# Kernel tuning notes

Measured on AMD Instinct MI355X. Metric: run time of the kernel, lower is better.

## Reference

```python
import jax, jax.numpy as jnp
import numpy as np

N = 50000          # nodes
E = 640000         # edges (before self-loops)
DIM_FEATS = 128
DIM_H = 32
HEADS1 = 8
NUM_CLASS = 16
NEG_SLOPE_ATT = 0.2   # PyG GATv2Conv default negative_slope
NEG_SLOPE_OUT = 0.01  # F.leaky_relu default


def setup_inputs() -> dict:
    key = jax.random.key(0)
    ks = jax.random.split(key, 12)
    s = 0.1
    x = jax.random.normal(ks[0], (N, DIM_FEATS), dtype=jnp.float32)
    edge_index = jax.random.randint(ks[1], (2, E), 0, N, dtype=jnp.int32)
    # GATv2Conv layer 1: dim_feats -> dim_h per head, 8 heads, concat
    W1l = jax.random.normal(ks[2], (DIM_FEATS, HEADS1 * DIM_H), dtype=jnp.float32) * s
    W1r = jax.random.normal(ks[3], (DIM_FEATS, HEADS1 * DIM_H), dtype=jnp.float32) * s
    att1 = jax.random.normal(ks[4], (HEADS1, DIM_H), dtype=jnp.float32) * s
    b1 = jnp.zeros((HEADS1 * DIM_H,), dtype=jnp.float32)
    # GATv2Conv layer 2: 256 -> num_class, 1 head, concat=False
    W2l = jax.random.normal(ks[5], (HEADS1 * DIM_H, NUM_CLASS), dtype=jnp.float32) * s
    W2r = jax.random.normal(ks[6], (HEADS1 * DIM_H, NUM_CLASS), dtype=jnp.float32) * s
    att2 = jax.random.normal(ks[7], (1, NUM_CLASS), dtype=jnp.float32) * s
    b2 = jnp.zeros((NUM_CLASS,), dtype=jnp.float32)
    return {"x": x, "edge_index": edge_index, "W1l": W1l, "W1r": W1r,
            "att1": att1, "b1": b1, "W2l": W2l, "W2r": W2r,
            "att2": att2, "b2": b2}


def _segment_softmax(scores, seg, num_segments):
    # scores: [E, H], seg: [E] destination node ids
    m = jax.ops.segment_max(scores, seg, num_segments=num_segments)  # [N, H]
    e = jnp.exp(scores - m[seg])
    denom = jax.ops.segment_sum(e, seg, num_segments=num_segments)   # [N, H]
    return e / (denom[seg] + 1e-16)


def _gatv2_layer(x, src, dst, Wl, Wr, att, bias, heads, out_ch, concat):
    n = x.shape[0]
    xl = (x @ Wl).reshape(n, heads, out_ch)  # source transform
    xr = (x @ Wr).reshape(n, heads, out_ch)  # target transform
    # per-edge GATv2 score: a^T LeakyReLU(xl[j] + xr[i])
    e = jax.nn.leaky_relu(xl[src] + xr[dst], negative_slope=NEG_SLOPE_ATT)  # [E,H,F]
    alpha = jnp.einsum('ehf,hf->eh', e, att)                                # [E,H]
    alpha = _segment_softmax(alpha, dst, n)
    msg = xl[src] * alpha[:, :, None]                                       # [E,H,F]
    out = jax.ops.segment_sum(msg, dst, num_segments=n)                     # [N,H,F]
    out = out.reshape(n, heads * out_ch) if concat else out.mean(axis=1)
    return out + bias


def reference(x, edge_index, W1l, W1r, att1, b1, W2l, W2r, att2, b2):
    # add_self_loops=True (PyG GATv2Conv default)
    loop = jnp.arange(N, dtype=edge_index.dtype)
    src = jnp.concatenate([edge_index[0], loop])
    dst = jnp.concatenate([edge_index[1], loop])
    # eval mode: all dropouts are identity
    h = _gatv2_layer(x, src, dst, W1l, W1r, att1, b1, HEADS1, DIM_H, concat=True)
    h = jax.nn.elu(h)
    h = _gatv2_layer(h, src, dst, W2l, W2r, att2, b2, 1, NUM_CLASS, concat=False)
    return jax.nn.leaky_relu(h, negative_slope=NEG_SLOPE_OUT)
```

## Files before the change

kernel.cpp:

```cpp
#include <hip/hip_runtime.h>
#include <math.h>

#define NN 50000
#define E0 640000
#define ET 690000
#define F1 128
#define D1 256
#define C2 16
#define NB 196
#define MPAD 50048
#define PADK 136
#define LOG2E 1.4426950408889634f
#define NBK1 782

typedef _Float16 f16x8 __attribute__((ext_vector_type(8)));
typedef _Float16 h2 __attribute__((ext_vector_type(2)));
typedef __attribute__((ext_vector_type(4))) float f32x4;

__device__ __forceinline__ unsigned short f2h(float f) {
  union { _Float16 h; unsigned short u; } c;
  c.h = (_Float16)f;
  return c.u;
}
__device__ __forceinline__ float h2f(unsigned short u) {
  union { unsigned short u; _Float16 h; } c; c.u = u; return (float)c.h;
}
__device__ __forceinline__ h2 u2h2(unsigned u) {
  union { unsigned u; h2 h; } c; c.u = u; return c.h;
}
__device__ __forceinline__ unsigned h22u(h2 h) {
  union { h2 h; unsigned u; } c; c.h = h; return c.u;
}

__global__ __launch_bounds__(256) void k_prep(
    const float* __restrict__ Wl, const float* __restrict__ Wr,
    const float* __restrict__ W2l, const float* __restrict__ W2r,
    const int* __restrict__ ei,
    unsigned short* __restrict__ wt, unsigned short* __restrict__ wt2,
    int* __restrict__ deg) {
  const int b = blockIdx.x;
  if (b < 256) {
    int tid = b * 256 + threadIdx.x;
    int n = tid >> 7, k = tid & 127;
    float v = (n < 256) ? Wl[k * 256 + n] : Wr[k * 256 + (n - 256)];
    wt[tid] = f2h(v);
  } else if (b < 288) {
    int tid = (b - 256) * 256 + threadIdx.x;
    int n = tid >> 8, k = tid & 255;
    float v = (n < 16) ? W2l[k * 16 + n] : W2r[k * 16 + (n - 16)];
    wt2[tid] = f2h(v);
  } else {
    int e = (b - 288) * 256 + threadIdx.x;
    if (e >= ET) return;
    int d = (e < E0) ? ei[E0 + e] : (e - E0);
    atomicAdd(&deg[d], 1);
  }
}

__global__ __launch_bounds__(256) void k_gemm1m(
    const float* __restrict__ x, const unsigned short* __restrict__ wt,
    unsigned short* __restrict__ xlh, unsigned short* __restrict__ xrh) {
  __shared__ unsigned short Al[128 * PADK];
  __shared__ unsigned short Bl[128 * PADK];
  const int t = threadIdx.x;
  const int m0 = blockIdx.x * 128;
  const int n0 = blockIdx.y * 128;
  {
    const int r = t >> 4;
    const int c = (t & 15) * 8;
#pragma unroll
    for (int p = 0; p < 8; ++p) {
      const int row = r + p * 16;
      const int rg = m0 + row;
      const float* xp = &x[(size_t)(rg < NN ? rg : NN - 1) * F1 + c];
      float4 lo = *(const float4*)xp;
      float4 hi = *(const float4*)(xp + 4);
      h2 q0 = h2{(_Float16)lo.x, (_Float16)lo.y};
      h2 q1 = h2{(_Float16)lo.z, (_Float16)lo.w};
      h2 q2 = h2{(_Float16)hi.x, (_Float16)hi.y};
      h2 q3 = h2{(_Float16)hi.z, (_Float16)hi.w};
      uint4 st; st.x = h22u(q0); st.y = h22u(q1); st.z = h22u(q2); st.w = h22u(q3);
      *(uint4*)&Al[row * PADK + c] = st;
      *(float4*)&Bl[row * PADK + c] = *(const float4*)&wt[(size_t)(n0 + row) * F1 + c];
    }
  }
  __syncthreads();
  const int wave = t >> 6, lane = t & 63;
  const int mw = (wave >> 1) * 64, nw = (wave & 1) * 64;
  const int fr = lane & 15, fq = lane >> 4;
  f32x4 acc[4][4] = {};
#pragma unroll
  for (int ks = 0; ks < 4; ++ks) {
    const int ko = ks * 32 + fq * 8;
    f16x8 a[4], b[4];
#pragma unroll
    for (int i = 0; i < 4; ++i)
      a[i] = *(const f16x8*)&Al[(mw + i * 16 + fr) * PADK + ko];
#pragma unroll
    for (int j = 0; j < 4; ++j)
      b[j] = *(const f16x8*)&Bl[(nw + j * 16 + fr) * PADK + ko];
#pragma unroll
    for (int i = 0; i < 4; ++i)
#pragma unroll
      for (int j = 0; j < 4; ++j)
        acc[i][j] = __builtin_amdgcn_mfma_f32_16x16x32_f16(a[i], b[j], acc[i][j], 0, 0, 0);
  }
  unsigned short* outp = (n0 < 256) ? xlh : xrh;
  const int cb = (n0 & 255) + nw + fr;
#pragma unroll
  for (int j = 0; j < 4; ++j) {
    const int col = cb + j * 16;
    const int head = col >> 5, f = col & 31;
    unsigned short* hp = outp + (size_t)head * NN * 32 + f;
#pragma unroll
    for (int i = 0; i < 4; ++i) {
      const int gm0 = m0 + mw + i * 16 + fq * 4;
#pragma unroll
      for (int r = 0; r < 4; ++r) {
        const int gm = gm0 + r;
        if (gm < NN) hp[(size_t)gm * 32] = f2h(acc[i][j][r]);
      }
    }
  }
}

__global__ __launch_bounds__(256) void k_scan_part(const int* __restrict__ deg,
                                                   int* __restrict__ part) {
  int i = blockIdx.x * 256 + threadIdx.x;
  int v = (i < NN) ? deg[i] : 0;
  v += __shfl_xor(v, 1);  v += __shfl_xor(v, 2);  v += __shfl_xor(v, 4);
  v += __shfl_xor(v, 8);  v += __shfl_xor(v, 16); v += __shfl_xor(v, 32);
  __shared__ int w[4];
  if ((threadIdx.x & 63) == 0) w[threadIdx.x >> 6] = v;
  __syncthreads();
  if (threadIdx.x == 0) part[blockIdx.x] = w[0] + w[1] + w[2] + w[3];
}

__global__ __launch_bounds__(256) void k_scan_apply(int* __restrict__ deg,
                                                    const int* __restrict__ part,
                                                    int* __restrict__ offs) {
  __shared__ int lds[256];
  __shared__ int red[4];
  const int b = blockIdx.x, t = threadIdx.x;
  const int i = b * 256 + t;
  int v = (i < NN) ? deg[i] : 0;
  lds[t] = v;
  int pp = 0;
  for (int j = t; j < b; j += 256) pp += part[j];
  pp += __shfl_xor(pp, 1);  pp += __shfl_xor(pp, 2);  pp += __shfl_xor(pp, 4);
  pp += __shfl_xor(pp, 8);  pp += __shfl_xor(pp, 16); pp += __shfl_xor(pp, 32);
  if ((t & 63) == 0) red[t >> 6] = pp;
  __syncthreads();
  const int prefix = red[0] + red[1] + red[2] + red[3];
  for (int off = 1; off < 256; off <<= 1) {
    int u = (t >= off) ? lds[t - off] : 0;
    __syncthreads();
    lds[t] += u;
    __syncthreads();
  }
  int excl = prefix + lds[t] - v;
  if (i < NN) { offs[i] = excl; deg[i] = excl; }
  if (b == NB - 1 && t == 255) offs[NN] = prefix + lds[255];
}

__global__ void k_scatter(const int* __restrict__ ei, int* __restrict__ cur,
                          unsigned short* __restrict__ csr) {
  int e = blockIdx.x * 256 + threadIdx.x;
  if (e >= ET) return;
  int s, d;
  if (e < E0) { s = ei[e]; d = ei[E0 + e]; } else { s = d = e - E0; }
  int pos = atomicAdd(&cur[d], 1);
  csr[pos] = (unsigned short)s;
}

__global__ __launch_bounds__(256) void k_agg1(
    const unsigned short* __restrict__ xlh, const unsigned short* __restrict__ xrh,
    unsigned short* __restrict__ hb,
    const int* __restrict__ offs, const unsigned short* __restrict__ csr,
    const float* __restrict__ att, const float* __restrict__ b1) {
  const int b = blockIdx.x;
  const int head = b & 7;
  const int wave = threadIdx.x >> 6;
  const int lane = threadIdx.x & 63;
  const int g = lane >> 2;
  const int j4 = lane & 3;
  const int n = (b >> 3) * 64 + wave * 16 + g;
  const bool valid = n < NN;
  const int colh = j4 * 8;
  const int col = head * 32 + colh;
  const unsigned short* xlhead = xlh + (size_t)head * NN * 32;

  const int nc = valid ? n : 0;
  const uint4 xru = *(const uint4*)&xrh[((size_t)head * NN + nc) * 32 + colh];
  h2 xr2[4];
  xr2[0] = u2h2(xru.x); xr2[1] = u2h2(xru.y);
  xr2[2] = u2h2(xru.z); xr2[3] = u2h2(xru.w);
  float at8[8];
  *(float4*)&at8[0] = *(const float4*)&att[col];
  *(float4*)&at8[4] = *(const float4*)&att[col + 4];
  h2 ath6[4], ath4[4];
#pragma unroll
  for (int j = 0; j < 4; ++j) {
    ath6[j] = h2{(_Float16)(at8[2 * j] * (0.6f * LOG2E)),
                 (_Float16)(at8[2 * j + 1] * (0.6f * LOG2E))};
    ath4[j] = h2{(_Float16)(at8[2 * j] * (0.4f * LOG2E)),
                 (_Float16)(at8[2 * j + 1] * (0.4f * LOG2E))};
  }
  float l = 0.f;
  h2 acc2[4] = {h2{0, 0}, h2{0, 0}, h2{0, 0}, h2{0, 0}};
  const int beg = valid ? offs[n] : 0;
  const int fin = valid ? offs[n + 1] : 0;

  auto score = [&](const h2* xh) -> float {
    float cv = 0.f, ca = 0.f;
#pragma unroll
    for (int j = 0; j < 4; ++j) {
      h2 v = xh[j] + xr2[j];
      h2 a = u2h2(h22u(v) & 0x7FFF7FFFu);
      cv = __builtin_amdgcn_fdot2(v, ath6[j], cv, false);
      ca = __builtin_amdgcn_fdot2(a, ath4[j], ca, false);
    }
    float c = cv + ca;
    c += __shfl_xor(c, 1);
    c += __shfl_xor(c, 2);
    return c;
  };

  int idx = beg;
  for (; idx + 1 < fin; idx += 2) {
    const int s0 = csr[idx], s1 = csr[idx + 1];
    const uint4 w0 = *(const uint4*)&xlhead[(size_t)s0 * 32 + colh];
    const uint4 w1 = *(const uint4*)&xlhead[(size_t)s1 * 32 + colh];
    h2 xh0[4], xh1[4];
    xh0[0] = u2h2(w0.x); xh0[1] = u2h2(w0.y); xh0[2] = u2h2(w0.z); xh0[3] = u2h2(w0.w);
    xh1[0] = u2h2(w1.x); xh1[1] = u2h2(w1.y); xh1[2] = u2h2(w1.z); xh1[3] = u2h2(w1.w);
    const float c0 = score(xh0);
    const float c1 = score(xh1);
    const float p0 = exp2f(c0), p1 = exp2f(c1);
    l += p0 + p1;
    const _Float16 p0h = (_Float16)p0, p1h = (_Float16)p1;
    const h2 p02 = h2{p0h, p0h}, p12 = h2{p1h, p1h};
#pragma unroll
    for (int j = 0; j < 4; ++j) acc2[j] += p02 * xh0[j] + p12 * xh1[j];
  }
  if (idx < fin) {
    const int s0 = csr[idx];
    const uint4 w0 = *(const uint4*)&xlhead[(size_t)s0 * 32 + colh];
    h2 xh0[4];
    xh0[0] = u2h2(w0.x); xh0[1] = u2h2(w0.y); xh0[2] = u2h2(w0.z); xh0[3] = u2h2(w0.w);
    const float c0 = score(xh0);
    const float p0 = exp2f(c0);
    l += p0;
    const _Float16 p0h = (_Float16)p0;
    const h2 p02 = h2{p0h, p0h};
#pragma unroll
    for (int j = 0; j < 4; ++j) acc2[j] += p02 * xh0[j];
  }
  if (valid) {
    const float rl = 1.f / (l + 1e-16f);
    float b8[8], o[8];
    *(float4*)&b8[0] = *(const float4*)&b1[col];
    *(float4*)&b8[4] = *(const float4*)&b1[col + 4];
#pragma unroll
    for (int j = 0; j < 4; ++j) {
      o[2 * j]     = (float)acc2[j][0] * rl + b8[2 * j];
      o[2 * j + 1] = (float)acc2[j][1] * rl + b8[2 * j + 1];
    }
#pragma unroll
    for (int k = 0; k < 8; ++k) o[k] = o[k] > 0.f ? o[k] : expm1f(o[k]);
    ushort4 p;
    p.x = f2h(o[0]); p.y = f2h(o[1]); p.z = f2h(o[2]); p.w = f2h(o[3]);
    ushort4 q;
    q.x = f2h(o[4]); q.y = f2h(o[5]); q.z = f2h(o[6]); q.w = f2h(o[7]);
    uint4 packed;
    packed.x = *(unsigned*)&p.x; packed.y = *(unsigned*)&p.z;
    packed.z = *(unsigned*)&q.x; packed.w = *(unsigned*)&q.z;
    *(uint4*)&hb[(size_t)n * D1 + col] = packed;
  }
}

__global__ __launch_bounds__(256) void k_gemm2m(
    const unsigned short* __restrict__ hb, const unsigned short* __restrict__ wt2,
    unsigned short* __restrict__ h2lh, float* __restrict__ h2r) {
  const int t = threadIdx.x;
  const int wave = t >> 6, lane = t & 63;
  const int fr = lane & 15, fq = lane >> 4;
  const int m0 = blockIdx.x * 128 + wave * 32;
  f32x4 acc[2][2] = {};
#pragma unroll
  for (int ks = 0; ks < 8; ++ks) {
    const int ko = ks * 32 + fq * 8;
    f16x8 a[2], b[2];
#pragma unroll
    for (int i = 0; i < 2; ++i) {
      int row = m0 + i * 16 + fr; if (row >= NN) row = NN - 1;
      a[i] = *(const f16x8*)&hb[(size_t)row * D1 + ko];
    }
#pragma unroll
    for (int j = 0; j < 2; ++j)
      b[j] = *(const f16x8*)&wt2[(j * 16 + fr) * 256 + ko];
#pragma unroll
    for (int i = 0; i < 2; ++i)
#pragma unroll
      for (int j = 0; j < 2; ++j)
        acc[i][j] = __builtin_amdgcn_mfma_f32_16x16x32_f16(a[i], b[j], acc[i][j], 0, 0, 0);
  }
#pragma unroll
  for (int i = 0; i < 2; ++i) {
    const int gm0 = m0 + i * 16 + fq * 4;
#pragma unroll
    for (int r = 0; r < 4; ++r) {
      const int gm = gm0 + r;
      if (gm < NN) {
        h2lh[(size_t)gm * C2 + fr] = f2h(acc[i][0][r]);
        h2r[(size_t)gm * C2 + fr] = acc[i][1][r];
      }
    }
  }
}

__global__ __launch_bounds__(256) void k_agg2(
    const unsigned short* __restrict__ h2lh, const float* __restrict__ h2r,
    const int* __restrict__ offs, const unsigned short* __restrict__ csr,
    const float* __restrict__ att2, const float* __restrict__ b2,
    float* __restrict__ out) {
  const int wave = threadIdx.x >> 6;
  const int lane = threadIdx.x & 63;
  const int n = blockIdx.x * 4 + wave;
  if (n >= NN) return;
  const int c = lane & 15, g = lane >> 4;
  const float xr_v = h2r[(size_t)n * C2 + c];
  const float att_v = att2[c] * LOG2E;
  float l = 0.f, acc = 0.f;
  const int beg = offs[n], fin = offs[n + 1];
  for (int idx = beg + g; idx < fin; idx += 4) {
    int s = csr[idx];
    float xlv = h2f(h2lh[(size_t)s * C2 + c]);
    float v = xlv + xr_v;
    v = fmaxf(v, 0.2f * v);
    float sc0 = v * att_v;
    sc0 += __shfl_xor(sc0, 1);
    sc0 += __shfl_xor(sc0, 2);
    sc0 += __shfl_xor(sc0, 4);
    sc0 += __shfl_xor(sc0, 8);
    float p = exp2f(sc0);
    l += p;
    acc = fmaf(p, xlv, acc);
  }
  l += __shfl_xor(l, 16);   l += __shfl_xor(l, 32);
  acc += __shfl_xor(acc, 16); acc += __shfl_xor(acc, 32);
  float o = acc / (l + 1e-16f) + b2[c];
  o = o > 0.f ? o : 0.01f * o;
  if (lane < 16) out[(size_t)n * C2 + c] = o;
}

extern "C" void kernel_launch(void* const* d_in, const int* in_sizes, int n_in,
                              void* d_out, int out_size, void* d_ws, size_t ws_size,
                              hipStream_t stream) {
  const float* x    = (const float*)d_in[0];
  const int*   ei   = (const int*)d_in[1];
  const float* W1l  = (const float*)d_in[2];
  const float* W1r  = (const float*)d_in[3];
  const float* att1 = (const float*)d_in[4];
  const float* b1   = (const float*)d_in[5];
  const float* W2l  = (const float*)d_in[6];
  const float* W2r  = (const float*)d_in[7];
  const float* att2 = (const float*)d_in[8];
  const float* b2   = (const float*)d_in[9];
  float* out = (float*)d_out;

  unsigned short* xlh = (unsigned short*)d_ws;
  unsigned short* xrh = xlh + (size_t)NN * D1;
  unsigned short* hb  = xrh + (size_t)NN * D1;
  int* deg  = (int*)(hb + (size_t)NN * D1);
  int* part = deg + NN;
  int* offs = part + NB;
  unsigned short* csr = (unsigned short*)(offs + NN + 1);
  unsigned short* wt  = csr + ET + 2;
  unsigned short* wt2 = wt + 512 * F1;
  unsigned short* h2lh = xlh;
  float* h2r = (float*)(h2lh + (size_t)NN * C2);

  hipMemsetAsync(deg, 0, NN * sizeof(int), stream);
  k_prep<<<288 + (ET + 255) / 256, 256, 0, stream>>>(
      W1l, W1r, W2l, W2r, ei, wt, wt2, deg);
  k_gemm1m<<<dim3(MPAD / 128, 4), 256, 0, stream>>>(x, wt, xlh, xrh);
  k_scan_part<<<NB, 256, 0, stream>>>(deg, part);
  k_scan_apply<<<NB, 256, 0, stream>>>(deg, part, offs);
  k_scatter<<<(ET + 255) / 256, 256, 0, stream>>>(ei, deg, csr);
  k_agg1<<<NBK1 * 8, 256, 0, stream>>>(xlh, xrh, hb, offs, csr, att1, b1);
  k_gemm2m<<<(NN + 127) / 128, 256, 0, stream>>>(hb, wt2, h2lh, h2r);
  k_agg2<<<NN / 4, 256, 0, stream>>>(h2lh, h2r, offs, csr, att2, b2, out);
}
```

Before: 271.6 us.

## Restructure gemm1 tiling, software-pipeline agg1 gathers, use DPP reductions

The first GEMM now uses 64-row tiles and each block loops over all four 128-column slices, so every x row is converted to fp16 only once instead of four times. The layer-1 aggregation switches to a 4-edge software-pipelined loop that prefetches the next group's feature gathers while computing the current group. Both aggregation kernels replace shuffle-based lane reductions with DPP adds, and layer 2 unrolls its edge loop by two. The GEMM change reloads the B slice four times per block, and the deeper pipeline raises register use, which may reduce occupancy.

After: 259.3 us. 1.05x faster.

```diff
diff --git a/kernel.cpp b/kernel.cpp
--- a/kernel.cpp
+++ b/kernel.cpp
@@ -30,6 +30,12 @@
 }
 __device__ __forceinline__ unsigned h22u(h2 h) {
   union { h2 h; unsigned u; } c; c.h = h; return c.u;
+}
+
+template <int CTRL>
+__device__ __forceinline__ float dpp_add(float c) {
+  int t = __builtin_amdgcn_update_dpp(0, __builtin_bit_cast(int, c), CTRL, 0xF, 0xF, true);
+  return c + __builtin_bit_cast(float, t);
 }
 
 __global__ __launch_bounds__(256) void k_prep(
@@ -60,16 +66,15 @@
 __global__ __launch_bounds__(256) void k_gemm1m(
     const float* __restrict__ x, const unsigned short* __restrict__ wt,
     unsigned short* __restrict__ xlh, unsigned short* __restrict__ xrh) {
-  __shared__ unsigned short Al[128 * PADK];
+  __shared__ unsigned short Al[64 * PADK];
   __shared__ unsigned short Bl[128 * PADK];
   const int t = threadIdx.x;
-  const int m0 = blockIdx.x * 128;
-  const int n0 = blockIdx.y * 128;
+  const int m0 = blockIdx.x * 64;
   {
     const int r = t >> 4;
     const int c = (t & 15) * 8;
 #pragma unroll
-    for (int p = 0; p < 8; ++p) {
+    for (int p = 0; p < 4; ++p) {
       const int row = r + p * 16;
       const int rg = m0 + row;
       const float* xp = &x[(size_t)(rg < NN ? rg : NN - 1) * F1 + c];
@@ -81,44 +86,56 @@
       h2 q3 = h2{(_Float16)hi.z, (_Float16)hi.w};
       uint4 st; st.x = h22u(q0); st.y = h22u(q1); st.z = h22u(q2); st.w = h22u(q3);
       *(uint4*)&Al[row * PADK + c] = st;
-      *(float4*)&Bl[row * PADK + c] = *(const float4*)&wt[(size_t)(n0 + row) * F1 + c];
-    }
-  }
-  __syncthreads();
+    }
+  }
   const int wave = t >> 6, lane = t & 63;
-  const int mw = (wave >> 1) * 64, nw = (wave & 1) * 64;
+  const int mw = (wave >> 1) * 32, nw = (wave & 1) * 64;
   const int fr = lane & 15, fq = lane >> 4;
-  f32x4 acc[4][4] = {};
-#pragma unroll
-  for (int ks = 0; ks < 4; ++ks) {
-    const int ko = ks * 32 + fq * 8;
-    f16x8 a[4], b[4];
-#pragma unroll
-    for (int i = 0; i < 4; ++i)
-      a[i] = *(const f16x8*)&Al[(mw + i * 16 + fr) * PADK + ko];
-#pragma unroll
-    for (int j = 0; j < 4; ++j)
-      b[j] = *(const f16x8*)&Bl[(nw + j * 16 + fr) * PADK + ko];
-#pragma unroll
-    for (int i = 0; i < 4; ++i)
+  for (int ny = 0; ny < 4; ++ny) {
+    const int n0 = ny * 128;
+    {
+      const int r = t >> 4;
+      const int c = (t & 15) * 8;
+#pragma unroll
+      for (int p = 0; p < 8; ++p) {
+        const int row = r + p * 16;
+        *(float4*)&Bl[row * PADK + c] = *(const float4*)&wt[(size_t)(n0 + row) * F1 + c];
+      }
+    }
+    __syncthreads();
+    f32x4 acc[2][4] = {};
+#pragma unroll
+    for (int ks = 0; ks < 4; ++ks) {
+      const int ko = ks * 32 + fq * 8;
+      f16x8 a[2], b[4];
+#pragma unroll
+      for (int i = 0; i < 2; ++i)
+        a[i] = *(const f16x8*)&Al[(mw + i * 16 + fr) * PADK + ko];
 #pragma unroll
       for (int j = 0; j < 4; ++j)
-        acc[i][j] = __builtin_amdgcn_mfma_f32_16x16x32_f16(a[i], b[j], acc[i][j], 0, 0, 0);
-  }
-  unsigned short* outp = (n0 < 256) ? xlh : xrh;
-  const int cb = (n0 & 255) + nw + fr;
-#pragma unroll
-  for (int j = 0; j < 4; ++j) {
-    const int col = cb + j * 16;
-    const int head = col >> 5, f = col & 31;
-    unsigned short* hp = outp + (size_t)head * NN * 32 + f;
-#pragma unroll
-    for (int i = 0; i < 4; ++i) {
-      const int gm0 = m0 + mw + i * 16 + fq * 4;
-#pragma unroll
-      for (int r = 0; r < 4; ++r) {
-        const int gm = gm0 + r;
-        if (gm < NN) hp[(size_t)gm * 32] = f2h(acc[i][j][r]);
+        b[j] = *(const f16x8*)&Bl[(nw + j * 16 + fr) * PADK + ko];
+#pragma unroll
+      for (int i = 0; i < 2; ++i)
+#pragma unroll
+        for (int j = 0; j < 4; ++j)
+          acc[i][j] = __builtin_amdgcn_mfma_f32_16x16x32_f16(a[i], b[j], acc[i][j], 0, 0, 0);
+    }
+    __syncthreads();
+    unsigned short* outp = (n0 < 256) ? xlh : xrh;
+    const int cb = (n0 & 255) + nw + fr;
+#pragma unroll
+    for (int j = 0; j < 4; ++j) {
+      const int col = cb + j * 16;
+      const int head = col >> 5, f = col & 31;
+      unsigned short* hp = outp + (size_t)head * NN * 32 + f;
+#pragma unroll
+      for (int i = 0; i < 2; ++i) {
+        const int gm0 = m0 + mw + i * 16 + fq * 4;
+#pragma unroll
+        for (int r = 0; r < 4; ++r) {
+          const int gm = gm0 + r;
+          if (gm < NN) hp[(size_t)gm * 32] = f2h(acc[i][j][r]);
+        }
       }
     }
   }
@@ -184,14 +201,14 @@
   const int lane = threadIdx.x & 63;
   const int g = lane >> 2;
   const int j4 = lane & 3;
-  const int n = (b >> 3) * 64 + wave * 16 + g;
-  const bool valid = n < NN;
+  const int idxn = (b >> 3) * 64 + wave * 16 + g;
+  const bool valid = idxn < NN;
+  const int n = valid ? idxn : 0;
   const int colh = j4 * 8;
   const int col = head * 32 + colh;
   const unsigned short* xlhead = xlh + (size_t)head * NN * 32;
 
-  const int nc = valid ? n : 0;
-  const uint4 xru = *(const uint4*)&xrh[((size_t)head * NN + nc) * 32 + colh];
+  const uint4 xru = *(const uint4*)&xrh[((size_t)head * NN + n) * 32 + colh];
   h2 xr2[4];
   xr2[0] = u2h2(xru.x); xr2[1] = u2h2(xru.y);
   xr2[2] = u2h2(xru.z); xr2[3] = u2h2(xru.w);
@@ -211,7 +228,12 @@
   const int beg = valid ? offs[n] : 0;
   const int fin = valid ? offs[n + 1] : 0;
 
-  auto score = [&](const h2* xh) -> float {
+  auto XL = [&](int s) -> uint4 {
+    return *(const uint4*)&xlhead[(size_t)s * 32 + colh];
+  };
+  auto edge = [&](const uint4& w) {
+    h2 xh[4];
+    xh[0] = u2h2(w.x); xh[1] = u2h2(w.y); xh[2] = u2h2(w.z); xh[3] = u2h2(w.w);
     float cv = 0.f, ca = 0.f;
 #pragma unroll
     for (int j = 0; j < 4; ++j) {
@@ -221,41 +243,41 @@
       ca = __builtin_amdgcn_fdot2(a, ath4[j], ca, false);
     }
     float c = cv + ca;
-    c += __shfl_xor(c, 1);
-    c += __shfl_xor(c, 2);
-    return c;
+    c = dpp_add<0xB1>(c);
+    c = dpp_add<0x4E>(c);
+    const float p = exp2f(c);
+    l += p;
+    const _Float16 ph = (_Float16)p;
+    const h2 p2 = h2{ph, ph};
+#pragma unroll
+    for (int j = 0; j < 4; ++j) acc2[j] += p2 * xh[j];
   };
 
   int idx = beg;
-  for (; idx + 1 < fin; idx += 2) {
-    const int s0 = csr[idx], s1 = csr[idx + 1];
-    const uint4 w0 = *(const uint4*)&xlhead[(size_t)s0 * 32 + colh];
-    const uint4 w1 = *(const uint4*)&xlhead[(size_t)s1 * 32 + colh];
-    h2 xh0[4], xh1[4];
-    xh0[0] = u2h2(w0.x); xh0[1] = u2h2(w0.y); xh0[2] = u2h2(w0.z); xh0[3] = u2h2(w0.w);
-    xh1[0] = u2h2(w1.x); xh1[1] = u2h2(w1.y); xh1[2] = u2h2(w1.z); xh1[3] = u2h2(w1.w);
-    const float c0 = score(xh0);
-    const float c1 = score(xh1);
-    const float p0 = exp2f(c0), p1 = exp2f(c1);
-    l += p0 + p1;
-    const _Float16 p0h = (_Float16)p0, p1h = (_Float16)p1;
-    const h2 p02 = h2{p0h, p0h}, p12 = h2{p1h, p1h};
-#pragma unroll
-    for (int j = 0; j < 4; ++j) acc2[j] += p02 * xh0[j] + p12 * xh1[j];
-  }
-  if (idx < fin) {
-    const int s0 = csr[idx];
-    const uint4 w0 = *(const uint4*)&xlhead[(size_t)s0 * 32 + colh];
-    h2 xh0[4];
-    xh0[0] = u2h2(w0.x); xh0[1] = u2h2(w0.y); xh0[2] = u2h2(w0.z); xh0[3] = u2h2(w0.w);
-    const float c0 = score(xh0);
-    const float p0 = exp2f(c0);
-    l += p0;
-    const _Float16 p0h = (_Float16)p0;
-    const h2 p02 = h2{p0h, p0h};
-#pragma unroll
-    for (int j = 0; j < 4; ++j) acc2[j] += p02 * xh0[j];
-  }
+  if (idx + 3 < fin) {
+    int s0 = csr[idx], s1 = csr[idx + 1], s2 = csr[idx + 2], s3 = csr[idx + 3];
+    uint4 w0 = XL(s0), w1 = XL(s1), w2 = XL(s2), w3 = XL(s3);
+    for (;;) {
+      const int nx = idx + 4;
+      const bool more = nx + 3 < fin;
+      const int b0 = more ? nx : beg;
+      const int b1i = more ? nx + 1 : beg;
+      const int b2i = more ? nx + 2 : beg;
+      const int b3i = more ? nx + 3 : beg;
+      const int t0 = csr[b0], t1 = csr[b1i], t2 = csr[b2i], t3 = csr[b3i];
+      const uint4 v0 = XL(t0), v1 = XL(t1), v2 = XL(t2), v3 = XL(t3);
+      edge(w0); edge(w1); edge(w2); edge(w3);
+      idx = nx;
+      if (!more) break;
+      w0 = v0; w1 = v1; w2 = v2; w3 = v3;
+    }
+  }
+  for (; idx < fin; ++idx) {
+    const int s = csr[idx];
+    const uint4 w = XL(s);
+    edge(w);
+  }
+
   if (valid) {
     const float rl = 1.f / (l + 1e-16f);
     float b8[8], o[8];
@@ -333,19 +355,24 @@
   const float att_v = att2[c] * LOG2E;
   float l = 0.f, acc = 0.f;
   const int beg = offs[n], fin = offs[n + 1];
-  for (int idx = beg + g; idx < fin; idx += 4) {
-    int s = csr[idx];
-    float xlv = h2f(h2lh[(size_t)s * C2 + c]);
-    float v = xlv + xr_v;
-    v = fmaxf(v, 0.2f * v);
-    float sc0 = v * att_v;
-    sc0 += __shfl_xor(sc0, 1);
-    sc0 += __shfl_xor(sc0, 2);
-    sc0 += __shfl_xor(sc0, 4);
-    sc0 += __shfl_xor(sc0, 8);
-    float p = exp2f(sc0);
-    l += p;
-    acc = fmaf(p, xlv, acc);
+  for (int idx = beg + g; idx < fin; idx += 8) {
+    const int i1 = idx + 4;
+    const bool m1 = i1 < fin;
+    const int s0 = csr[idx];
+    const int s1 = csr[m1 ? i1 : idx];
+    const float xl0 = h2f(h2lh[(size_t)s0 * C2 + c]);
+    const float xl1 = h2f(h2lh[(size_t)s1 * C2 + c]);
+    float v0 = xl0 + xr_v; v0 = fmaxf(v0, 0.2f * v0);
+    float v1 = xl1 + xr_v; v1 = fmaxf(v1, 0.2f * v1);
+    float sc0 = v0 * att_v, sc1 = v1 * att_v;
+    sc0 = dpp_add<0xB1>(sc0);   sc1 = dpp_add<0xB1>(sc1);
+    sc0 = dpp_add<0x4E>(sc0);   sc1 = dpp_add<0x4E>(sc1);
+    sc0 = dpp_add<0x124>(sc0);  sc1 = dpp_add<0x124>(sc1);
+    sc0 = dpp_add<0x128>(sc0);  sc1 = dpp_add<0x128>(sc1);
+    const float p0 = exp2f(sc0);
+    const float p1 = m1 ? exp2f(sc1) : 0.f;
+    l += p0 + p1;
+    acc = fmaf(p0, xl0, fmaf(p1, xl1, acc));
   }
   l += __shfl_xor(l, 16);   l += __shfl_xor(l, 32);
   acc += __shfl_xor(acc, 16); acc += __shfl_xor(acc, 32);
@@ -384,7 +411,7 @@
   hipMemsetAsync(deg, 0, NN * sizeof(int), stream);
   k_prep<<<288 + (ET + 255) / 256, 256, 0, stream>>>(
       W1l, W1r, W2l, W2r, ei, wt, wt2, deg);
-  k_gemm1m<<<dim3(MPAD / 128, 4), 256, 0, stream>>>(x, wt, xlh, xrh);
+  k_gemm1m<<<MPAD / 64, 256, 0, stream>>>(x, wt, xlh, xrh);
   k_scan_part<<<NB, 256, 0, stream>>>(deg, part);
   k_scan_apply<<<NB, 256, 0, stream>>>(deg, part, offs);
   k_scatter<<<(ET + 255) / 256, 256, 0, stream>>>(ei, deg, csr);
```
